# Kernel tuning notes

Hardware: AMD Instinct MI355X
Metric: run time of the kernel (lower is better)

The kernel has to match this reference:

```python
import jax, jax.numpy as jnp
import numpy as np

EPS = 1e-8  # torch cosine_similarity eps


def setup_inputs() -> dict:
    key = jax.random.key(0)
    kx, kw = jax.random.split(key)
    B, D, C, K = 512, 512, 5994, 3
    x = jax.random.normal(kx, (B, D), dtype=jnp.float32)
    # xavier_normal over (D, C, K): std = sqrt(2 / (fan_in + fan_out))
    std = float(np.sqrt(2.0 / (D + C * K)))
    W = jax.random.normal(kw, (D, C, K), dtype=jnp.float32) * std
    return {"x": x, "W": W}


def reference(x, W):
    # cosine similarity along feature dim, without materializing [B, D, C, K]
    x_norm = jnp.maximum(jnp.linalg.norm(x, axis=1, keepdims=True), EPS)   # [B, 1]
    w_norm = jnp.maximum(jnp.linalg.norm(W, axis=0, keepdims=True), EPS)   # [1, C, K]
    xn = x / x_norm                                                        # [B, D]
    Wn = W / w_norm                                                        # [D, C, K]
    costh = jnp.einsum('bd,dck->bck', xn, Wn)                              # [B, C, K]
    return costh
```

## Files before the change

kernel.cpp:

```cpp
#include <hip/hip_runtime.h>
#include <hip/hip_bf16.h>
#include <stdint.h>


#define D_DIM 512
#define BM 128
#define BN 128
#define NG (D_DIM / 8)
#define NSTEPS (D_DIM / 32)
#define TILE_BYTES (NG * BM * 16)

typedef __bf16 bf16x8 __attribute__((ext_vector_type(8)));
typedef float f32x4 __attribute__((ext_vector_type(4)));

__device__ __forceinline__ unsigned short f2bf(float f) {
  union { float f; unsigned int u; } v; v.f = f;
  unsigned int u = v.u;
  u += 0x7fffu + ((u >> 16) & 1u);
  return (unsigned short)(u >> 16);
}

__device__ __forceinline__ void load_lds16(const void* g, void* l) {
  __builtin_amdgcn_global_load_lds(
      (__attribute__((address_space(1))) void*)(g),
      (__attribute__((address_space(3))) void*)(l), 16, 0, 0);
}

__global__ void xnorm_kernel(const float* __restrict__ x, unsigned short* __restrict__ An) {
  const int m = blockIdx.x;
  const int t = threadIdx.x;
  const float* xr = x + (size_t)m * D_DIM + t * 8;
  float4 a = *(const float4*)(xr);
  float4 b = *(const float4*)(xr + 4);
  float s = a.x * a.x + a.y * a.y + a.z * a.z + a.w * a.w +
            b.x * b.x + b.y * b.y + b.z * b.z + b.w * b.w;
#pragma unroll
  for (int off = 32; off; off >>= 1) s += __shfl_xor(s, off, 64);
  const float inv = 1.f / fmaxf(sqrtf(s), 1e-8f);
  ushort4 o0, o1;
  o0.x = f2bf(a.x * inv); o0.y = f2bf(a.y * inv); o0.z = f2bf(a.z * inv); o0.w = f2bf(a.w * inv);
  o1.x = f2bf(b.x * inv); o1.y = f2bf(b.y * inv); o1.z = f2bf(b.z * inv); o1.w = f2bf(b.w * inv);
  const int mtile = m >> 7, r = m & 127;
  unsigned short* dst = An + (size_t)mtile * (TILE_BYTES / 2) + (size_t)t * (BM * 8) + r * 8;
  *(ushort4*)dst = o0;
  *(ushort4*)(dst + 4) = o1;
}

__global__ void wtrans2_kernel(const float* __restrict__ W, unsigned short* __restrict__ Wt,
                               float* __restrict__ partial, int CK, int NT128) {
  __shared__ unsigned short tile[64][128];
  __shared__ float red[256 * 4];
  const int t = threadIdx.x;
  const int ntile = blockIdx.x, gb = blockIdx.y;
  const int n0 = ntile * BN;
  const int cq = t & 31;
  const int dr = t >> 5;
  const int d_base = gb * 64;
  float ss0 = 0.f, ss1 = 0.f, ss2 = 0.f, ss3 = 0.f;

  if (n0 + BN <= CK) {
#pragma unroll
    for (int i = 0; i < 8; ++i) {
      const int dl = dr + i * 8;
      float4 v = *(const float4*)(W + (size_t)(d_base + dl) * CK + n0 + cq * 4);
      ss0 += v.x * v.x; ss1 += v.y * v.y; ss2 += v.z * v.z; ss3 += v.w * v.w;
      ushort4 o; o.x = f2bf(v.x); o.y = f2bf(v.y); o.z = f2bf(v.z); o.w = f2bf(v.w);
      *(ushort4*)&tile[dl][cq * 4] = o;
    }
  } else {
#pragma unroll
    for (int i = 0; i < 8; ++i) {
      const int dl = dr + i * 8;
      float v[4];
#pragma unroll
      for (int e = 0; e < 4; ++e) {
        int n = n0 + cq * 4 + e;
        v[e] = W[(size_t)(d_base + dl) * CK + (n < CK ? n : CK - 1)];
      }
      ss0 += v[0] * v[0]; ss1 += v[1] * v[1]; ss2 += v[2] * v[2]; ss3 += v[3] * v[3];
      ushort4 o; o.x = f2bf(v[0]); o.y = f2bf(v[1]); o.z = f2bf(v[2]); o.w = f2bf(v[3]);
      *(ushort4*)&tile[dl][cq * 4] = o;
    }
  }
  red[t * 4 + 0] = ss0; red[t * 4 + 1] = ss1; red[t * 4 + 2] = ss2; red[t * 4 + 3] = ss3;
  __syncthreads();

  if (t < 128) {
    float s = 0.f;
#pragma unroll
    for (int k = 0; k < 8; ++k) s += red[k * 128 + t];
    partial[(size_t)gb * NT128 + n0 + t] = s;
  }

  unsigned short* outBase = Wt + (size_t)ntile * (TILE_BYTES / 2);
#pragma unroll
  for (int i = 0; i < 4; ++i) {
    const int idx = t + 256 * i;
    const int g = idx >> 7, r = idx & 127;
    ushort4 o0, o1;
    o0.x = tile[g * 8 + 0][r]; o0.y = tile[g * 8 + 1][r];
    o0.z = tile[g * 8 + 2][r]; o0.w = tile[g * 8 + 3][r];
    o1.x = tile[g * 8 + 4][r]; o1.y = tile[g * 8 + 5][r];
    o1.z = tile[g * 8 + 6][r]; o1.w = tile[g * 8 + 7][r];
    unsigned short* dst = outBase + (size_t)(gb * 8 + g) * (BM * 8) + r * 8;
    *(ushort4*)dst = o0;
    *(ushort4*)(dst + 4) = o1;
  }
}

__global__ __launch_bounds__(256, 2) void gemm_kernel(const unsigned short* __restrict__ An,
                                                      const unsigned short* __restrict__ Wt,
                                                      const float* __restrict__ partial,
                                                      float* __restrict__ out, int CK, int NT128) {
  __shared__ __attribute__((aligned(16))) unsigned char lds[16384];
  unsigned char* ldsA = lds;
  unsigned char* ldsB = lds + 8192;
  const int ntile = blockIdx.x, mtile = blockIdx.y;
  const int t = threadIdx.x;
  const int lane = t & 63, w = t >> 6;
  const int wm = w >> 1, wn = w & 1;
  const int lrow = lane & 15;
  const int g = lane >> 4;

  const unsigned char* srcA = (const unsigned char*)An + (size_t)mtile * TILE_BYTES;
  const unsigned char* srcB = (const unsigned char*)Wt + (size_t)ntile * TILE_BYTES;

  f32x4 acc[4][4] = {};

  for (int kt = 0; kt < NSTEPS; ++kt) {
    const size_t koff = (size_t)kt * 8192;
#pragma unroll
    for (int c = 0; c < 2; ++c) {
      const int off = w * 2048 + c * 1024;
      load_lds16(srcA + koff + off + lane * 16, ldsA + off);
      load_lds16(srcB + koff + off + lane * 16, ldsB + off);
    }
    __syncthreads();
    bf16x8 afrag[4], bfrag[4];
#pragma unroll
    for (int i = 0; i < 4; ++i) {
      afrag[i] = *(const bf16x8*)(ldsA + g * 2048 + (wm * 64 + i * 16 + lrow) * 16);
      bfrag[i] = *(const bf16x8*)(ldsB + g * 2048 + (wn * 64 + i * 16 + lrow) * 16);
    }
#pragma unroll
    for (int i = 0; i < 4; ++i)
#pragma unroll
      for (int j = 0; j < 4; ++j)
        acc[i][j] = __builtin_amdgcn_mfma_f32_16x16x32_bf16(afrag[i], bfrag[j], acc[i][j], 0, 0, 0);
    __syncthreads();
  }

  float* winv = (float*)lds;
  if (t < 128) {
    float s = 0.f;
#pragma unroll
    for (int k = 0; k < 8; ++k) s += partial[(size_t)k * NT128 + ntile * BN + t];
    winv[t] = 1.f / fmaxf(sqrtf(s), 1e-8f);
  }
  __syncthreads();

#pragma unroll
  for (int j = 0; j < 4; ++j) {
    const int cl = wn * 64 + j * 16 + lrow;
    const int col = ntile * BN + cl;
    if (col < CK) {
      const float wv = winv[cl];
#pragma unroll
      for (int i = 0; i < 4; ++i) {
#pragma unroll
        for (int jj = 0; jj < 4; ++jj) {
          const int row = mtile * BM + wm * 64 + i * 16 + g * 4 + jj;
          out[(size_t)row * CK + col] = acc[i][j][jj] * wv;
        }
      }
    }
  }
}

extern "C" void kernel_launch(void* const* d_in, const int* in_sizes, int n_in,
                              void* d_out, int out_size, void* d_ws, size_t ws_size,
                              hipStream_t stream) {
  const float* x = (const float*)d_in[0];
  const float* W = (const float*)d_in[1];
  float* out = (float*)d_out;
  const int Bn = in_sizes[0] / D_DIM;
  const int CK = in_sizes[1] / D_DIM;
  const int ntiles = (CK + BN - 1) / BN;
  const int mtiles = Bn / BM;
  const int NT128 = ntiles * BN;

  unsigned char* ws = (unsigned char*)d_ws;
  float* partial = (float*)ws;
  unsigned short* An = (unsigned short*)(ws + 655360);
  unsigned short* Wt = (unsigned short*)(ws + 655360 + (size_t)mtiles * TILE_BYTES);

  hipLaunchKernelGGL(xnorm_kernel, dim3(Bn), dim3(64), 0, stream, x, An);
  hipLaunchKernelGGL(wtrans2_kernel, dim3(ntiles, 8), dim3(256), 0, stream, W, Wt, partial, CK, NT128);
  hipLaunchKernelGGL(gemm_kernel, dim3(ntiles, mtiles), dim3(256), 0, stream, An, Wt, partial, out, CK, NT128);
}
```

Measured before the change: 42.89 us.

## Fuse W conversion and column norms into GEMM with double-buffered LDS pipeline

Removes the separate W transpose/convert kernel and its workspace round trip. The GEMM now reads fp32 W columns directly, converts them to bf16 into LDS, accumulates column squared norms in registers, and double-buffers both A and B tiles with register prefetch and manual waitcnt/barrier control. The xnorm kernel also packs four rows per block. In exchange, each of the four M-tile blocks re-reads and re-converts the same W columns. The per-thread column-strided global loads may coalesce less well than the old transpose path.

```diff
diff --git a/kernel.cpp b/kernel.cpp
--- a/kernel.cpp
+++ b/kernel.cpp
@@ -6,12 +6,12 @@
 #define D_DIM 512
 #define BM 128
 #define BN 128
-#define NG (D_DIM / 8)
-#define NSTEPS (D_DIM / 32)
-#define TILE_BYTES (NG * BM * 16)
+#define NSTEPS 16
+#define TILE_BYTES (64 * BM * 16)
 
 typedef __bf16 bf16x8 __attribute__((ext_vector_type(8)));
 typedef float f32x4 __attribute__((ext_vector_type(4)));
+typedef unsigned short ushort8 __attribute__((ext_vector_type(8)));
 
 __device__ __forceinline__ unsigned short f2bf(float f) {
   union { float f; unsigned int u; } v; v.f = f;
@@ -27,9 +27,10 @@
 }
 
 __global__ void xnorm_kernel(const float* __restrict__ x, unsigned short* __restrict__ An) {
-  const int m = blockIdx.x;
   const int t = threadIdx.x;
-  const float* xr = x + (size_t)m * D_DIM + t * 8;
+  const int w = t >> 6, lane = t & 63;
+  const int m = blockIdx.x * 4 + w;
+  const float* xr = x + (size_t)m * D_DIM + lane * 8;
   float4 a = *(const float4*)(xr);
   float4 b = *(const float4*)(xr + 4);
   float s = a.x * a.x + a.y * a.y + a.z * a.z + a.w * a.w +
@@ -41,120 +42,105 @@
   o0.x = f2bf(a.x * inv); o0.y = f2bf(a.y * inv); o0.z = f2bf(a.z * inv); o0.w = f2bf(a.w * inv);
   o1.x = f2bf(b.x * inv); o1.y = f2bf(b.y * inv); o1.z = f2bf(b.z * inv); o1.w = f2bf(b.w * inv);
   const int mtile = m >> 7, r = m & 127;
-  unsigned short* dst = An + (size_t)mtile * (TILE_BYTES / 2) + (size_t)t * (BM * 8) + r * 8;
+  unsigned short* dst = An + (size_t)mtile * (TILE_BYTES / 2) + (size_t)lane * (BM * 8) + r * 8;
   *(ushort4*)dst = o0;
   *(ushort4*)(dst + 4) = o1;
 }
 
-__global__ void wtrans2_kernel(const float* __restrict__ W, unsigned short* __restrict__ Wt,
-                               float* __restrict__ partial, int CK, int NT128) {
-  __shared__ unsigned short tile[64][128];
-  __shared__ float red[256 * 4];
-  const int t = threadIdx.x;
-  const int ntile = blockIdx.x, gb = blockIdx.y;
-  const int n0 = ntile * BN;
-  const int cq = t & 31;
-  const int dr = t >> 5;
-  const int d_base = gb * 64;
-  float ss0 = 0.f, ss1 = 0.f, ss2 = 0.f, ss3 = 0.f;
-
-  if (n0 + BN <= CK) {
-#pragma unroll
-    for (int i = 0; i < 8; ++i) {
-      const int dl = dr + i * 8;
-      float4 v = *(const float4*)(W + (size_t)(d_base + dl) * CK + n0 + cq * 4);
-      ss0 += v.x * v.x; ss1 += v.y * v.y; ss2 += v.z * v.z; ss3 += v.w * v.w;
-      ushort4 o; o.x = f2bf(v.x); o.y = f2bf(v.y); o.z = f2bf(v.z); o.w = f2bf(v.w);
-      *(ushort4*)&tile[dl][cq * 4] = o;
-    }
-  } else {
-#pragma unroll
-    for (int i = 0; i < 8; ++i) {
-      const int dl = dr + i * 8;
-      float v[4];
-#pragma unroll
-      for (int e = 0; e < 4; ++e) {
-        int n = n0 + cq * 4 + e;
-        v[e] = W[(size_t)(d_base + dl) * CK + (n < CK ? n : CK - 1)];
-      }
-      ss0 += v[0] * v[0]; ss1 += v[1] * v[1]; ss2 += v[2] * v[2]; ss3 += v[3] * v[3];
-      ushort4 o; o.x = f2bf(v[0]); o.y = f2bf(v[1]); o.z = f2bf(v[2]); o.w = f2bf(v[3]);
-      *(ushort4*)&tile[dl][cq * 4] = o;
-    }
-  }
-  red[t * 4 + 0] = ss0; red[t * 4 + 1] = ss1; red[t * 4 + 2] = ss2; red[t * 4 + 3] = ss3;
-  __syncthreads();
-
-  if (t < 128) {
-    float s = 0.f;
-#pragma unroll
-    for (int k = 0; k < 8; ++k) s += red[k * 128 + t];
-    partial[(size_t)gb * NT128 + n0 + t] = s;
-  }
-
-  unsigned short* outBase = Wt + (size_t)ntile * (TILE_BYTES / 2);
-#pragma unroll
-  for (int i = 0; i < 4; ++i) {
-    const int idx = t + 256 * i;
-    const int g = idx >> 7, r = idx & 127;
-    ushort4 o0, o1;
-    o0.x = tile[g * 8 + 0][r]; o0.y = tile[g * 8 + 1][r];
-    o0.z = tile[g * 8 + 2][r]; o0.w = tile[g * 8 + 3][r];
-    o1.x = tile[g * 8 + 4][r]; o1.y = tile[g * 8 + 5][r];
-    o1.z = tile[g * 8 + 6][r]; o1.w = tile[g * 8 + 7][r];
-    unsigned short* dst = outBase + (size_t)(gb * 8 + g) * (BM * 8) + r * 8;
-    *(ushort4*)dst = o0;
-    *(ushort4*)(dst + 4) = o1;
-  }
-}
-
-__global__ __launch_bounds__(256, 2) void gemm_kernel(const unsigned short* __restrict__ An,
-                                                      const unsigned short* __restrict__ Wt,
-                                                      const float* __restrict__ partial,
-                                                      float* __restrict__ out, int CK, int NT128) {
-  __shared__ __attribute__((aligned(16))) unsigned char lds[16384];
-  unsigned char* ldsA = lds;
-  unsigned char* ldsB = lds + 8192;
+__global__ __launch_bounds__(256, 2) void gemm_fused(const unsigned short* __restrict__ An,
+                                                     const float* __restrict__ W,
+                                                     float* __restrict__ out, int CK) {
+  __shared__ __attribute__((aligned(16))) unsigned char lds[32768];
   const int ntile = blockIdx.x, mtile = blockIdx.y;
   const int t = threadIdx.x;
   const int lane = t & 63, w = t >> 6;
   const int wm = w >> 1, wn = w & 1;
   const int lrow = lane & 15;
-  const int g = lane >> 4;
+  const int kg = lane >> 4;
 
   const unsigned char* srcA = (const unsigned char*)An + (size_t)mtile * TILE_BYTES;
-  const unsigned char* srcB = (const unsigned char*)Wt + (size_t)ntile * TILE_BYTES;
+  const int n0 = ntile * BN;
+  const int nn = t & 127;
+  const int h = t >> 7;
+  const int ncl = (n0 + nn < CK) ? nn : (CK - 1 - n0);
+  const float* __restrict__ Wcol = W + n0 + ncl;
 
   f32x4 acc[4][4] = {};
+  float wsq = 0.f;
+  float r[16];
 
+#pragma unroll
+  for (int l = 0; l < 16; ++l)
+    r[l] = Wcol[(size_t)((h + 2 * (l >> 3)) * 8 + (l & 7)) * CK];
+#pragma unroll
+  for (int c = 0; c < 2; ++c) {
+    const int off = w * 2048 + c * 1024;
+    load_lds16(srcA + off + lane * 16, lds + off);
+  }
+
+#pragma unroll 2
   for (int kt = 0; kt < NSTEPS; ++kt) {
-    const size_t koff = (size_t)kt * 8192;
+    const int cur = kt & 1;
+    unsigned char* bufA = lds + cur * 8192;
+    unsigned char* bufB = lds + 16384 + cur * 8192;
+
 #pragma unroll
-    for (int c = 0; c < 2; ++c) {
-      const int off = w * 2048 + c * 1024;
-      load_lds16(srcA + koff + off + lane * 16, ldsA + off);
-      load_lds16(srcB + koff + off + lane * 16, ldsB + off);
+    for (int idx = 0; idx < 2; ++idx) {
+      bf16x8 v;
+#pragma unroll
+      for (int j = 0; j < 8; ++j) {
+        const float f = r[idx * 8 + j];
+        wsq += f * f;
+        v[j] = (__bf16)f;
+      }
+      *(bf16x8*)(bufB + (h + 2 * idx) * 2048 + nn * 16) = v;
     }
-    __syncthreads();
+
+    if (kt + 1 < NSTEPS) {
+#pragma unroll
+      for (int l = 0; l < 16; ++l)
+        r[l] = Wcol[(size_t)((kt + 1) * 32 + (h + 2 * (l >> 3)) * 8 + (l & 7)) * CK];
+    }
+
+    __builtin_amdgcn_sched_barrier(0);
+    if (kt + 1 < NSTEPS) {
+      asm volatile("s_waitcnt vmcnt(16)" ::: "memory");
+    } else {
+      asm volatile("s_waitcnt vmcnt(0)" ::: "memory");
+    }
+    asm volatile("s_waitcnt lgkmcnt(0)" ::: "memory");
+    __builtin_amdgcn_s_barrier();
+    __builtin_amdgcn_sched_barrier(0);
+
+    if (kt + 1 < NSTEPS) {
+      unsigned char* bufAn = lds + (cur ^ 1) * 8192;
+      const size_t koff = (size_t)(kt + 1) * 8192;
+#pragma unroll
+      for (int c = 0; c < 2; ++c) {
+        const int off = w * 2048 + c * 1024;
+        load_lds16(srcA + koff + off + lane * 16, bufAn + off);
+      }
+    }
+
     bf16x8 afrag[4], bfrag[4];
 #pragma unroll
     for (int i = 0; i < 4; ++i) {
-      afrag[i] = *(const bf16x8*)(ldsA + g * 2048 + (wm * 64 + i * 16 + lrow) * 16);
-      bfrag[i] = *(const bf16x8*)(ldsB + g * 2048 + (wn * 64 + i * 16 + lrow) * 16);
+      afrag[i] = *(const bf16x8*)(bufA + kg * 2048 + (wm * 64 + i * 16 + lrow) * 16);
+      bfrag[i] = *(const bf16x8*)(bufB + kg * 2048 + (wn * 64 + i * 16 + lrow) * 16);
     }
 #pragma unroll
     for (int i = 0; i < 4; ++i)
 #pragma unroll
       for (int j = 0; j < 4; ++j)
         acc[i][j] = __builtin_amdgcn_mfma_f32_16x16x32_bf16(afrag[i], bfrag[j], acc[i][j], 0, 0, 0);
-    __syncthreads();
   }
 
-  float* winv = (float*)lds;
+  float* red = (float*)lds;
+  float* winv = (float*)(lds + 2048);
+  red[t] = wsq;
+  __syncthreads();
   if (t < 128) {
-    float s = 0.f;
-#pragma unroll
-    for (int k = 0; k < 8; ++k) s += partial[(size_t)k * NT128 + ntile * BN + t];
+    const float s = red[t] + red[t + 128];
     winv[t] = 1.f / fmaxf(sqrtf(s), 1e-8f);
   }
   __syncthreads();
@@ -162,14 +148,14 @@
 #pragma unroll
   for (int j = 0; j < 4; ++j) {
     const int cl = wn * 64 + j * 16 + lrow;
-    const int col = ntile * BN + cl;
+    const int col = n0 + cl;
     if (col < CK) {
       const float wv = winv[cl];
 #pragma unroll
       for (int i = 0; i < 4; ++i) {
 #pragma unroll
         for (int jj = 0; jj < 4; ++jj) {
-          const int row = mtile * BM + wm * 64 + i * 16 + g * 4 + jj;
+          const int row = mtile * BM + wm * 64 + i * 16 + kg * 4 + jj;
           out[(size_t)row * CK + col] = acc[i][j][jj] * wv;
         }
       }
@@ -187,14 +173,9 @@
   const int CK = in_sizes[1] / D_DIM;
   const int ntiles = (CK + BN - 1) / BN;
   const int mtiles = Bn / BM;
-  const int NT128 = ntiles * BN;
 
-  unsigned char* ws = (unsigned char*)d_ws;
-  float* partial = (float*)ws;
-  unsigned short* An = (unsigned short*)(ws + 655360);
-  unsigned short* Wt = (unsigned short*)(ws + 655360 + (size_t)mtiles * TILE_BYTES);
+  unsigned short* An = (unsigned short*)d_ws;
 
-  hipLaunchKernelGGL(xnorm_kernel, dim3(Bn), dim3(64), 0, stream, x, An);
-  hipLaunchKernelGGL(wtrans2_kernel, dim3(ntiles, 8), dim3(256), 0, stream, W, Wt, partial, CK, NT128);
-  hipLaunchKernelGGL(gemm_kernel, dim3(ntiles, mtiles), dim3(256), 0, stream, An, Wt, partial, out, CK, NT128);
+  hipLaunchKernelGGL(xnorm_kernel, dim3(Bn / 4), dim3(256), 0, stream, x, An);
+  hipLaunchKernelGGL(gemm_fused, dim3(ntiles, mtiles), dim3(256), 0, stream, An, W, out, CK);
 }
```

Result: slower. 52.79 us (+23.1%).
